# Kernel tuning notes

Hardware: AMD Instinct MI355X
Metric: run time of the kernel (lower is better)

Reference implementation:

```python
import jax, jax.numpy as jnp
import numpy as np
import math

B, S, E, H, F, L, V = 4, 256, 512, 8, 2048, 4, 32000
HD = E // H
MAXLEN = 5000  # EnhancedPositionalEncoding max_len default


def _ln(x, s, b):
    m = jnp.mean(x, axis=-1, keepdims=True)
    v = jnp.mean((x - m) ** 2, axis=-1, keepdims=True)
    return (x - m) / jnp.sqrt(v + 1e-5) * s + b


def setup_inputs() -> dict:
    key = jax.random.key(0)
    ks = jax.random.split(key, 10)
    n = lambda k, shape: jax.random.normal(k, shape, jnp.float32) * 0.02
    return {
        "src": jax.random.randint(ks[0], (B, S), 0, V),
        "emb": jax.random.uniform(ks[1], (V, E), jnp.float32, -0.1, 0.1),
        "rel_table": n(ks[2], (2 * MAXLEN - 1, E)),
        "norm_in_s": jnp.ones(E, jnp.float32), "norm_in_b": jnp.zeros(E, jnp.float32),
        "inW": n(ks[3], (L, 3 * E, E)), "inB": jnp.zeros((L, 3 * E), jnp.float32),
        "outW": n(ks[4], (L, E, E)), "outB": jnp.zeros((L, E), jnp.float32),
        "ln1_s": jnp.ones((L, E), jnp.float32), "ln1_b": jnp.zeros((L, E), jnp.float32),
        "ln2_s": jnp.ones((L, E), jnp.float32), "ln2_b": jnp.zeros((L, E), jnp.float32),
        "w1": n(ks[5], (L, F, E)), "b1": jnp.zeros((L, F), jnp.float32),
        "w2": n(ks[6], (L, E, F)), "b2": jnp.zeros((L, E), jnp.float32),
        "normf_s": jnp.ones(E, jnp.float32), "normf_b": jnp.zeros(E, jnp.float32),
        "dec_w": jax.random.uniform(ks[7], (V, E), jnp.float32, -0.1, 0.1),
        "dec_b": jnp.zeros(V, jnp.float32),
    }


def reference(src, emb, rel_table, norm_in_s, norm_in_b, inW, inB, outW, outB,
              ln1_s, ln1_b, ln2_s, ln2_b, w1, b1, w2, b2, normf_s, normf_b,
              dec_w, dec_b):
    x = emb[src] * math.sqrt(E)                 # [B,S,E], pos_encoder is identity in relative mode
    x = _ln(x, norm_in_s, norm_in_b)
    # relative-position embedding gather: idx[l,m] = (m - l) + S - 1
    pos = jnp.arange(S)
    rel_idx = (pos[None, :] - pos[:, None]) + S - 1
    rel = rel_table[rel_idx].reshape(S, S, H, HD)  # [S,S,H,hd]
    # NOTE: torch adds the BOOL triu mask to float scores -> +1.0 at masked positions
    mask = jnp.triu(jnp.ones((S, S), jnp.float32), 1)
    scale = 1.0 / math.sqrt(HD)
    for l in range(L):
        h = _ln(x, ln1_s[l], ln1_b[l])
        qkv = h @ inW[l].T + inB[l]
        q, k, v = jnp.split(qkv, 3, axis=-1)
        q = q.reshape(B, S, H, HD).transpose(0, 2, 1, 3)  # [B,H,S,hd]
        k = k.reshape(B, S, H, HD).transpose(0, 2, 1, 3)
        v = v.reshape(B, S, H, HD).transpose(0, 2, 1, 3)
        scores = jnp.einsum('bhqd,bhkd->bhqk', q, k) * scale
        bias = jnp.einsum('bhld,lmhd->bhlm', q, rel)      # relative-position bias (unscaled, as in torch)
        attn = jax.nn.softmax(scores + bias + mask, axis=-1)
        o = jnp.einsum('bhqk,bhkd->bhqd', attn, v).transpose(0, 2, 1, 3).reshape(B, S, E)
        x = x + (o @ outW[l].T + outB[l])
        h2 = _ln(x, ln2_s[l], ln2_b[l])
        ff = jax.nn.gelu(h2 @ w1[l].T + b1[l], approximate=False) @ w2[l].T + b2[l]
        x = x + ff
    x = _ln(x, normf_s, normf_b)  # encoder final norm
    return x @ dec_w.T + dec_b    # [B,S,V]
```

## Files before the change

kernel.cpp:

```cpp
#include <hip/hip_runtime.h>
#include <hip/hip_bf16.h>
#include <math.h>

#define BB 4
#define SS 256
#define EE 512
#define HH 8
#define HD 64
#define FFD 2048
#define LL 4
#define VV 32000
#define BS (BB*SS)
#define SQRT_E 22.627416997969522f
#define ATTN_SCALE 0.125f

typedef __bf16 bf16;
typedef __attribute__((ext_vector_type(4))) __bf16 bf16x4;
typedef __attribute__((ext_vector_type(8))) __bf16 bf16x8;
typedef __attribute__((ext_vector_type(4))) float f32x4;

#define GLOBAL_AS __attribute__((address_space(1)))
#define LDS_AS    __attribute__((address_space(3)))

__device__ __forceinline__ void load_lds16(const bf16* g, bf16* l) {
    __builtin_amdgcn_global_load_lds((const GLOBAL_AS unsigned int*)g,
                                     (LDS_AS unsigned int*)l, 16, 0, 0);
}

__global__ void cvt_all(const float* __restrict__ inW, const float* __restrict__ outW,
                        const float* __restrict__ w1, const float* __restrict__ w2,
                        const float* __restrict__ dec, const float* __restrict__ rel,
                        bf16* __restrict__ inWb, bf16* __restrict__ outWb,
                        bf16* __restrict__ w1b, bf16* __restrict__ w2b,
                        bf16* __restrict__ decb, bf16* __restrict__ relb,
                        const int* __restrict__ src, const float* __restrict__ emb,
                        const float* __restrict__ nsc, const float* __restrict__ nbi,
                        float* __restrict__ xout) {
    int b = blockIdx.x;
    int t = threadIdx.x;
    if (b >= 28544) {
        int row = b - 28544;
        const float* r = emb + (size_t)src[row] * EE;
        float v0 = r[t] * SQRT_E, v1 = r[t + 256] * SQRT_E;
        float sum = v0 + v1, sq = v0 * v0 + v1 * v1;
        #pragma unroll
        for (int off = 32; off; off >>= 1) {
            sum += __shfl_xor(sum, off);
            sq  += __shfl_xor(sq, off);
        }
        __shared__ float ssum[4], ssq[4];
        int wid = t >> 6, lane = t & 63;
        if (lane == 0) { ssum[wid] = sum; ssq[wid] = sq; }
        __syncthreads();
        sum = ssum[0] + ssum[1] + ssum[2] + ssum[3];
        sq  = ssq[0] + ssq[1] + ssq[2] + ssq[3];
        float mean = sum * (1.0f / EE);
        float var  = sq * (1.0f / EE) - mean * mean;
        float rstd = rsqrtf(var + 1e-5f);
        xout[(size_t)row * EE + t]       = (v0 - mean) * rstd * nsc[t] + nbi[t];
        xout[(size_t)row * EE + t + 256] = (v1 - mean) * rstd * nsc[t + 256] + nbi[t + 256];
        return;
    }
    const float* s; bf16* d; int base; int n;
    if (b < 3072)       { s = inW;  d = inWb;  base = b;         n = 3145728; }
    else if (b < 4096)  { s = outW; d = outWb; base = b - 3072;  n = 1048576; }
    else if (b < 8192)  { s = w1;   d = w1b;   base = b - 4096;  n = 4194304; }
    else if (b < 12288) { s = w2;   d = w2b;   base = b - 8192;  n = 4194304; }
    else if (b < 28288) { s = dec;  d = decb;  base = b - 12288; n = 16384000; }
    else                { s = rel;  d = relb;  base = b - 28288; n = 261632; }
    int i = (base * 256 + t) * 4;
    if (i < n) {
        float4 v = *(const float4*)(s + i);
        bf16x4 o;
        o[0] = (bf16)v.x; o[1] = (bf16)v.y; o[2] = (bf16)v.z; o[3] = (bf16)v.w;
        *(bf16x4*)(d + i) = o;
    }
}

template <typename OT>
__global__ void ln_kernel(const float* __restrict__ in, const float* __restrict__ sc,
                          const float* __restrict__ bi, OT* __restrict__ out) {
    int row = blockIdx.x;
    int t = threadIdx.x;
    const float* r = in + (size_t)row * EE;
    float v0 = r[t], v1 = r[t + 256];
    float sum = v0 + v1, sq = v0 * v0 + v1 * v1;
    #pragma unroll
    for (int off = 32; off; off >>= 1) {
        sum += __shfl_xor(sum, off);
        sq  += __shfl_xor(sq, off);
    }
    __shared__ float ssum[4], ssq[4];
    int wid = t >> 6, lane = t & 63;
    if (lane == 0) { ssum[wid] = sum; ssq[wid] = sq; }
    __syncthreads();
    sum = ssum[0] + ssum[1] + ssum[2] + ssum[3];
    sq  = ssq[0] + ssq[1] + ssq[2] + ssq[3];
    float mean = sum * (1.0f / EE);
    float var  = sq * (1.0f / EE) - mean * mean;
    float rstd = rsqrtf(var + 1e-5f);
    out[(size_t)row * EE + t]       = (OT)((v0 - mean) * rstd * sc[t] + bi[t]);
    out[(size_t)row * EE + t + 256] = (OT)((v1 - mean) * rstd * sc[t + 256] + bi[t + 256]);
}

__global__ void embed_ln_kernel(const int* __restrict__ src, const float* __restrict__ emb,
                                const float* __restrict__ sc, const float* __restrict__ bi,
                                float* __restrict__ out) {
    int row = blockIdx.x;
    int t = threadIdx.x;
    const float* r = emb + (size_t)src[row] * EE;
    float v0 = r[t] * SQRT_E, v1 = r[t + 256] * SQRT_E;
    float sum = v0 + v1, sq = v0 * v0 + v1 * v1;
    #pragma unroll
    for (int off = 32; off; off >>= 1) {
        sum += __shfl_xor(sum, off);
        sq  += __shfl_xor(sq, off);
    }
    __shared__ float ssum[4], ssq[4];
    int wid = t >> 6, lane = t & 63;
    if (lane == 0) { ssum[wid] = sum; ssq[wid] = sq; }
    __syncthreads();
    sum = ssum[0] + ssum[1] + ssum[2] + ssum[3];
    sq  = ssq[0] + ssq[1] + ssq[2] + ssq[3];
    float mean = sum * (1.0f / EE);
    float var  = sq * (1.0f / EE) - mean * mean;
    float rstd = rsqrtf(var + 1e-5f);
    out[(size_t)row * EE + t]       = (v0 - mean) * rstd * sc[t] + bi[t];
    out[(size_t)row * EE + t + 256] = (v1 - mean) * rstd * sc[t + 256] + bi[t + 256];
}

template <int BM, int BN, int MODE, int OBF16, int WRVT, int SWZ, int SPLITK>
__global__ __launch_bounds__(256) void gemm_bf16(
        const bf16* __restrict__ A, const bf16* __restrict__ W,
        const float* __restrict__ bias, void* __restrict__ Cout,
        const float* __restrict__ res, bf16* __restrict__ vT,
        int M, int N, int K) {
    constexpr int FM = BM / 32, FN = BN / 32;
    __shared__ bf16 Atile[2][BM * 32];
    __shared__ bf16 Btile[2][BN * 32];
    int tid = threadIdx.x;
    int wid = tid >> 6, lane = tid & 63;
    int wm = (wid >> 1) * (BM / 2), wn = (wid & 1) * (BN / 2);
    int bm, bn;
    if (SWZ) {
        int nbm = gridDim.x;
        int linear = blockIdx.y * nbm + blockIdx.x;
        int total = nbm * gridDim.y;
        int chunk = total >> 3;
        int xcd = linear & 7, idx = linear >> 3;
        int g = xcd * chunk + idx;
        bm = (g % nbm) * BM;
        bn = (g / nbm) * BN;
    } else {
        bm = blockIdx.x * BM;
        bn = blockIdx.y * BN;
    }
    int kp = (SPLITK > 1) ? blockIdx.z : 0;
    int kbeg = kp * (K / SPLITK);
    int kend = kbeg + K / SPLITK;

    f32x4 acc[FM][FN];
    #pragma unroll
    for (int i = 0; i < FM; i++)
        #pragma unroll
        for (int j = 0; j < FN; j++)
            acc[i][j] = (f32x4){0.f, 0.f, 0.f, 0.f};

    int mrow = lane & 15, kq = (lane >> 4) * 8;

    auto stage = [&](int buf, int k0) {
        #pragma unroll
        for (int it = 0; it < BM / 64; it++) {
            int c = it * 256 + tid;
            int row = c >> 2, kc = (c & 3) * 8;
            load_lds16(A + (size_t)(bm + row) * K + k0 + kc, &Atile[buf][c * 8]);
        }
        #pragma unroll
        for (int it = 0; it < BN / 64; it++) {
            int c = it * 256 + tid;
            int row = c >> 2, kc = (c & 3) * 8;
            load_lds16(W + (size_t)(bn + row) * K + k0 + kc, &Btile[buf][c * 8]);
        }
    };

    stage(0, kbeg);
    __syncthreads();
    int cur = 0;
    for (int k0 = kbeg; k0 < kend; k0 += 32) {
        if (k0 + 32 < kend) stage(cur ^ 1, k0 + 32);
        bf16x8 af[FM], bfv[FN];
        #pragma unroll
        for (int i = 0; i < FM; i++)
            af[i] = *(const bf16x8*)(&Atile[cur][(wm + i * 16 + mrow) * 32 + kq]);
        #pragma unroll
        for (int j = 0; j < FN; j++)
            bfv[j] = *(const bf16x8*)(&Btile[cur][(wn + j * 16 + mrow) * 32 + kq]);
        #pragma unroll
        for (int i = 0; i < FM; i++)
            #pragma unroll
            for (int j = 0; j < FN; j++)
                acc[i][j] = __builtin_amdgcn_mfma_f32_16x16x32_bf16(af[i], bfv[j], acc[i][j], 0, 0, 0);
        __syncthreads();
        cur ^= 1;
    }

    #pragma unroll
    for (int i = 0; i < FM; i++) {
        int row0 = bm + wm + i * 16 + (lane >> 4) * 4;
        #pragma unroll
        for (int j = 0; j < FN; j++) {
            int col = bn + wn + j * 16 + (lane & 15);
            float bv = bias[col];
            #pragma unroll
            for (int r = 0; r < 4; r++) {
                int row = row0 + r;
                if (SPLITK > 1) {
                    float v = acc[i][j][r];
                    if (kp == 0) v += bv;
                    atomicAdd((float*)Cout + (size_t)row * N + col, v);
                    continue;
                }
                float v = acc[i][j][r] + bv;
                if (MODE == 1) v = 0.5f * v * (1.0f + erff(v * 0.7071067811865476f));
                if (MODE == 2) v += res[(size_t)row * N + col];
                if (WRVT && col >= 1024) {
                    int cc = col - 1024;
                    vT[(size_t)(((row >> 8) * 8 + (cc >> 6)) * 64 + (cc & 63)) * 256 + (row & 255)] = (bf16)v;
                } else if (OBF16) ((bf16*)Cout)[(size_t)row * N + col] = (bf16)v;
                else              ((float*)Cout)[(size_t)row * N + col] = v;
            }
        }
    }
}

__global__ __launch_bounds__(256) void attn_mfma(const bf16* __restrict__ qkv,
        const bf16* __restrict__ relb, const bf16* __restrict__ vT,
        bf16* __restrict__ o) {
    int blk = blockIdx.x;
    int qt = blk & 3, bh = blk >> 2;
    int h = bh & 7, b = bh >> 3;
    int q0 = qt * 64, j0 = 192 - q0;
    int tid = threadIdx.x;
    int wid = tid >> 6, lane = tid & 63;
    int l15 = lane & 15, quad = lane >> 4;
    int mr0 = wid * 16;

    __shared__ __align__(16) bf16 Qs[64 * 72];
    __shared__ __align__(16) bf16 Stg[64 * 72];
    __shared__ __align__(16) bf16 BP[64 * 264];

    int c0 = tid, c1 = 256 + tid;
    int r0 = c0 >> 3, ch0 = (c0 & 7) * 8;
    int r1 = c1 >> 3, ch1 = (c1 & 7) * 8;

    const size_t qbase = (size_t)(b * 256 + q0) * 1536 + h * 64;
    *(bf16x8*)(Qs + r0 * 72 + ch0) = *(const bf16x8*)(qkv + qbase + (size_t)r0 * 1536 + ch0);
    *(bf16x8*)(Qs + r1 * 72 + ch1) = *(const bf16x8*)(qkv + qbase + (size_t)r1 * 1536 + ch1);

    bf16x8 pf0, pf1;
    {
        const size_t rb = (size_t)j0 * 512 + h * 64;
        pf0 = *(const bf16x8*)(relb + rb + (size_t)r0 * 512 + ch0);
        pf1 = *(const bf16x8*)(relb + rb + (size_t)r1 * 512 + ch1);
    }

    __syncthreads();
    bf16x8 af0 = *(const bf16x8*)(Qs + (mr0 + l15) * 72 + quad * 8);
    bf16x8 af1 = *(const bf16x8*)(Qs + (mr0 + l15) * 72 + 32 + quad * 8);

    f32x4 S[16];
    #pragma unroll
    for (int i = 0; i < 16; i++) S[i] = (f32x4){0.f, 0.f, 0.f, 0.f};

    for (int jc = 0; jc < 5; jc++) {
        *(bf16x8*)(Stg + r0 * 72 + ch0) = pf0;
        *(bf16x8*)(Stg + r1 * 72 + ch1) = pf1;
        __syncthreads();
        if (jc < 4) {
            const size_t rb = (size_t)(j0 + (jc + 1) * 64) * 512 + h * 64;
            pf0 = *(const bf16x8*)(relb + rb + (size_t)r0 * 512 + ch0);
            pf1 = *(const bf16x8*)(relb + rb + (size_t)r1 * 512 + ch1);
        } else {
            const size_t kb = (size_t)(b * 256) * 1536 + 512 + h * 64;
            pf0 = *(const bf16x8*)(qkv + kb + (size_t)r0 * 1536 + ch0);
            pf1 = *(const bf16x8*)(qkv + kb + (size_t)r1 * 1536 + ch1);
        }
        #pragma unroll
        for (int jt = 0; jt < 4; jt++) {
            f32x4 acc = (f32x4){0.f, 0.f, 0.f, 0.f};
            bf16x8 bv0 = *(const bf16x8*)(Stg + (jt * 16 + l15) * 72 + quad * 8);
            bf16x8 bv1 = *(const bf16x8*)(Stg + (jt * 16 + l15) * 72 + 32 + quad * 8);
            acc = __builtin_amdgcn_mfma_f32_16x16x32_bf16(af0, bv0, acc, 0, 0, 0);
            acc = __builtin_amdgcn_mfma_f32_16x16x32_bf16(af1, bv1, acc, 0, 0, 0);
            int jp = jc * 64 + jt * 16 + l15;
            #pragma unroll
            for (int r = 0; r < 4; r++) {
                int ll = mr0 + quad * 4 + r;
                int m = jp + ll - 63;
                if (m >= 0 && m < 256) BP[ll * 256 + m] = (bf16)acc[r];
            }
        }
        __syncthreads();
    }

    for (int kc = 0; kc < 4; kc++) {
        *(bf16x8*)(Stg + r0 * 72 + ch0) = pf0;
        *(bf16x8*)(Stg + r1 * 72 + ch1) = pf1;
        __syncthreads();
        if (kc < 3) {
            const size_t kb = (size_t)(b * 256 + (kc + 1) * 64) * 1536 + 512 + h * 64;
            pf0 = *(const bf16x8*)(qkv + kb + (size_t)r0 * 1536 + ch0);
            pf1 = *(const bf16x8*)(qkv + kb + (size_t)r1 * 1536 + ch1);
        } else {
            const size_t vb = (size_t)(bh * 64) * 256;
            pf0 = *(const bf16x8*)(vT + vb + (size_t)r0 * 256 + ch0);
            pf1 = *(const bf16x8*)(vT + vb + (size_t)r1 * 256 + ch1);
        }
        #pragma unroll
        for (int nt = 0; nt < 4; nt++) {
            bf16x8 bv0 = *(const bf16x8*)(Stg + (nt * 16 + l15) * 72 + quad * 8);
            bf16x8 bv1 = *(const bf16x8*)(Stg + (nt * 16 + l15) * 72 + 32 + quad * 8);
            S[kc * 4 + nt] = __builtin_amdgcn_mfma_f32_16x16x32_bf16(af0, bv0, S[kc * 4 + nt], 0, 0, 0);
            S[kc * 4 + nt] = __builtin_amdgcn_mfma_f32_16x16x32_bf16(af1, bv1, S[kc * 4 + nt], 0, 0, 0);
        }
        __syncthreads();
    }

    float rmax[4] = {-1e30f, -1e30f, -1e30f, -1e30f};
    #pragma unroll
    for (int T = 0; T < 16; T++) {
        int m = T * 16 + l15;
        #pragma unroll
        for (int r = 0; r < 4; r++) {
            int ll = mr0 + quad * 4 + r;
            float v = S[T][r] * ATTN_SCALE + (float)BP[ll * 256 + m]
                      + ((m > q0 + ll) ? 1.0f : 0.0f);
            S[T][r] = v;
            rmax[r] = fmaxf(rmax[r], v);
        }
    }
    #pragma unroll
    for (int r = 0; r < 4; r++)
        #pragma unroll
        for (int d = 1; d < 16; d <<= 1)
            rmax[r] = fmaxf(rmax[r], __shfl_xor(rmax[r], d));
    float rsum[4] = {0.f, 0.f, 0.f, 0.f};
    #pragma unroll
    for (int T = 0; T < 16; T++)
        #pragma unroll
        for (int r = 0; r < 4; r++) {
            float p = expf(S[T][r] - rmax[r]);
            S[T][r] = p;
            rsum[r] += p;
        }
    #pragma unroll
    for (int r = 0; r < 4; r++)
        #pragma unroll
        for (int d = 1; d < 16; d <<= 1)
            rsum[r] += __shfl_xor(rsum[r], d);

    __syncthreads();
    #pragma unroll
    for (int T = 0; T < 16; T++)
        #pragma unroll
        for (int r = 0; r < 4; r++)
            BP[(mr0 + quad * 4 + r) * 264 + T * 16 + l15] = (bf16)S[T][r];

    f32x4 oacc[4];
    #pragma unroll
    for (int i = 0; i < 4; i++) oacc[i] = (f32x4){0.f, 0.f, 0.f, 0.f};
    for (int kc = 0; kc < 4; kc++) {
        *(bf16x8*)(Stg + r0 * 72 + ch0) = pf0;
        *(bf16x8*)(Stg + r1 * 72 + ch1) = pf1;
        __syncthreads();
        if (kc < 3) {
            const size_t vb = (size_t)(bh * 64) * 256 + (kc + 1) * 64;
            pf0 = *(const bf16x8*)(vT + vb + (size_t)r0 * 256 + ch0);
            pf1 = *(const bf16x8*)(vT + vb + (size_t)r1 * 256 + ch1);
        }
        #pragma unroll
        for (int ks = 0; ks < 2; ks++) {
            bf16x8 ap = *(const bf16x8*)(BP + (mr0 + l15) * 264 + kc * 64 + ks * 32 + quad * 8);
            #pragma unroll
            for (int nt = 0; nt < 4; nt++) {
                bf16x8 bv = *(const bf16x8*)(Stg + (nt * 16 + l15) * 72 + ks * 32 + quad * 8);
                oacc[nt] = __builtin_amdgcn_mfma_f32_16x16x32_bf16(ap, bv, oacc[nt], 0, 0, 0);
            }
        }
        __syncthreads();
    }

    #pragma unroll
    for (int nt = 0; nt < 4; nt++)
        #pragma unroll
        for (int r = 0; r < 4; r++) {
            int ll = mr0 + quad * 4 + r;
            o[(size_t)(b * 256 + q0 + ll) * 512 + h * 64 + nt * 16 + l15] =
                (bf16)(oacc[nt][r] * (1.0f / rsum[r]));
        }
}

template <int MODE>
__global__ void gemm_nt(const float* __restrict__ A, const float* __restrict__ W,
                        const float* __restrict__ bias, float* __restrict__ C,
                        const float* __restrict__ res, int M, int N, int K) {
    __shared__ float As[64][17];
    __shared__ float Ws[64][17];
    int tid = threadIdx.x;
    int tx = tid & 15, ty = tid >> 4;
    int bm = blockIdx.y * 64, bn = blockIdx.x * 64;
    float acc[4][4] = {};
    for (int k0 = 0; k0 < K; k0 += 16) {
        #pragma unroll
        for (int i = 0; i < 4; i++) {
            int idx = tid + i * 256;
            int r = idx >> 4, c = idx & 15;
            As[r][c] = A[(size_t)(bm + r) * K + k0 + c];
            Ws[r][c] = W[(size_t)(bn + r) * K + k0 + c];
        }
        __syncthreads();
        #pragma unroll
        for (int kk = 0; kk < 16; kk++) {
            float a[4], w[4];
            #pragma unroll
            for (int i = 0; i < 4; i++) a[i] = As[ty * 4 + i][kk];
            #pragma unroll
            for (int j = 0; j < 4; j++) w[j] = Ws[tx * 4 + j][kk];
            #pragma unroll
            for (int i = 0; i < 4; i++)
                #pragma unroll
                for (int j = 0; j < 4; j++)
                    acc[i][j] += a[i] * w[j];
        }
        __syncthreads();
    }
    #pragma unroll
    for (int i = 0; i < 4; i++) {
        int row = bm + ty * 4 + i;
        #pragma unroll
        for (int j = 0; j < 4; j++) {
            int col = bn + tx * 4 + j;
            float v = acc[i][j] + bias[col];
            if (MODE == 1) v = 0.5f * v * (1.0f + erff(v * 0.7071067811865476f));
            if (MODE == 2) v += res[(size_t)row * N + col];
            C[(size_t)row * N + col] = v;
        }
    }
}

__global__ void attn_kernel(const float* __restrict__ qkv, const float* __restrict__ rel_table,
                            float* __restrict__ o) {
    int blk = blockIdx.x;
    int l = blk & (SS - 1);
    int bh = blk >> 8;
    int h = bh & (HH - 1);
    int b = bh >> 3;
    int t = threadIdx.x;
    int wid = t >> 6, lane = t & 63;

    __shared__ float qs[HD];
    __shared__ float attn_s[SS];
    __shared__ float swave[4];
    __shared__ float opart[4][HD];

    const float* qrow = qkv + (size_t)(b * SS + l) * (3 * EE) + h * HD;
    if (t < HD) qs[t] = qrow[t];
    __syncthreads();

    const float* krow   = qkv + (size_t)(b * SS + t) * (3 * EE) + EE + h * HD;
    const float* relrow = rel_table + (size_t)(t - l + SS - 1) * EE + h * HD;
    const float4* k4 = reinterpret_cast<const float4*>(krow);
    const float4* r4 = reinterpret_cast<const float4*>(relrow);
    float s1 = 0.f, s2 = 0.f;
    #pragma unroll
    for (int d4 = 0; d4 < HD / 4; d4++) {
        float4 kv = k4[d4], rv = r4[d4];
        float q0 = qs[4 * d4], q1 = qs[4 * d4 + 1], q2 = qs[4 * d4 + 2], q3 = qs[4 * d4 + 3];
        s1 += q0 * kv.x + q1 * kv.y + q2 * kv.z + q3 * kv.w;
        s2 += q0 * rv.x + q1 * rv.y + q2 * rv.z + q3 * rv.w;
    }
    float val = s1 * ATTN_SCALE + s2 + ((t > l) ? 1.0f : 0.0f);

    float m = val;
    #pragma unroll
    for (int off = 32; off; off >>= 1) m = fmaxf(m, __shfl_xor(m, off));
    if (lane == 0) swave[wid] = m;
    __syncthreads();
    m = fmaxf(fmaxf(swave[0], swave[1]), fmaxf(swave[2], swave[3]));
    float p = expf(val - m);
    float s = p;
    #pragma unroll
    for (int off = 32; off; off >>= 1) s += __shfl_xor(s, off);
    __syncthreads();
    if (lane == 0) swave[wid] = s;
    __syncthreads();
    float tot = swave[0] + swave[1] + swave[2] + swave[3];
    attn_s[t] = p;
    __syncthreads();

    int d = t & 63, part = t >> 6;
    const float* vbase = qkv + (size_t)(b * SS) * (3 * EE) + 2 * EE + h * HD + d;
    float acc = 0.f;
    int m0 = part * 64;
    #pragma unroll 8
    for (int mm = m0; mm < m0 + 64; mm++)
        acc += attn_s[mm] * vbase[(size_t)mm * (3 * EE)];
    opart[part][d] = acc;
    __syncthreads();
    if (t < 64) {
        float ov = (opart[0][d] + opart[1][d] + opart[2][d] + opart[3][d]) / tot;
        o[(size_t)(b * SS + l) * EE + h * HD + d] = ov;
    }
}

extern "C" void kernel_launch(void* const* d_in, const int* in_sizes, int n_in,
                              void* d_out, int out_size, void* d_ws, size_t ws_size,
                              hipStream_t stream) {
    const int*   src    = (const int*)  d_in[0];
    const float* emb    = (const float*)d_in[1];
    const float* rel    = (const float*)d_in[2];
    const float* nin_s  = (const float*)d_in[3];
    const float* nin_b  = (const float*)d_in[4];
    const float* inW    = (const float*)d_in[5];
    const float* inB    = (const float*)d_in[6];
    const float* outW   = (const float*)d_in[7];
    const float* outB   = (const float*)d_in[8];
    const float* ln1_s  = (const float*)d_in[9];
    const float* ln1_b  = (const float*)d_in[10];
    const float* ln2_s  = (const float*)d_in[11];
    const float* ln2_b  = (const float*)d_in[12];
    const float* w1     = (const float*)d_in[13];
    const float* b1     = (const float*)d_in[14];
    const float* w2     = (const float*)d_in[15];
    const float* b2     = (const float*)d_in[16];
    const float* normf_s= (const float*)d_in[17];
    const float* normf_b= (const float*)d_in[18];
    const float* dec_w  = (const float*)d_in[19];
    const float* dec_b  = (const float*)d_in[20];
    float* out = (float*)d_out;

    const size_t n_inW  = (size_t)LL * 3 * EE * EE;
    const size_t n_outW = (size_t)LL * EE * EE;
    const size_t n_w1   = (size_t)LL * FFD * EE;
    const size_t n_w2   = (size_t)LL * EE * FFD;
    const size_t n_dec  = (size_t)VV * EE;

    float* x    = (float*)d_ws;
    bf16*  qkvb = (bf16*)(x + (size_t)BS * EE);
    bf16*  hb   = qkvb + (size_t)BS * 3 * EE;
    bf16*  ob   = hb + (size_t)BS * EE;
    bf16*  ffb  = ob + (size_t)BS * EE;
    bf16*  vTb  = ffb + (size_t)BS * FFD;
    bf16*  relb = vTb + (size_t)BS * 512;
    bf16*  inWb  = relb + (size_t)512 * EE;
    bf16*  outWb = inWb + n_inW;
    bf16*  w1b   = outWb + n_outW;
    bf16*  w2b   = w1b + n_w1;
    bf16*  decWb = w2b + n_w2;
    size_t needed = (size_t)((char*)(decWb + n_dec) - (char*)d_ws);

    if (ws_size >= needed) {
        cvt_all<<<29568, 256, 0, stream>>>(inW, outW, w1, w2, dec_w, rel,
                                           inWb, outWb, w1b, w2b, decWb, relb,
                                           src, emb, nin_s, nin_b, x);

        for (int l = 0; l < LL; l++) {
            ln_kernel<bf16><<<BS, 256, 0, stream>>>(x, ln1_s + l * EE, ln1_b + l * EE, hb);
            gemm_bf16<64, 64, 0, 1, 1, 1, 1><<<dim3(BS / 64, 3 * EE / 64), 256, 0, stream>>>(
                hb, inWb + (size_t)l * 3 * EE * EE, inB + (size_t)l * 3 * EE, qkvb, nullptr,
                vTb, BS, 3 * EE, EE);
            attn_mfma<<<BB * HH * 4, 256, 0, stream>>>(qkvb, relb, vTb, ob);
            gemm_bf16<64, 64, 2, 0, 0, 1, 2><<<dim3(BS / 64, EE / 64, 2), 256, 0, stream>>>(
                ob, outWb + (size_t)l * EE * EE, outB + (size_t)l * EE, x, x,
                nullptr, BS, EE, EE);
            ln_kernel<bf16><<<BS, 256, 0, stream>>>(x, ln2_s + l * EE, ln2_b + l * EE, hb);
            gemm_bf16<64, 64, 1, 1, 0, 1, 1><<<dim3(BS / 64, FFD / 64), 256, 0, stream>>>(
                hb, w1b + (size_t)l * FFD * EE, b1 + (size_t)l * FFD, ffb, nullptr,
                nullptr, BS, FFD, EE);
            gemm_bf16<64, 64, 2, 0, 0, 1, 4><<<dim3(BS / 64, EE / 64, 4), 256, 0, stream>>>(
                ffb, w2b + (size_t)l * EE * FFD, b2 + (size_t)l * EE, x, x,
                nullptr, BS, EE, FFD);
        }

        ln_kernel<bf16><<<BS, 256, 0, stream>>>(x, normf_s, normf_b, hb);
        gemm_bf16<128, 128, 0, 0, 0, 1, 1><<<dim3(BS / 128, VV / 128), 256, 0, stream>>>(
            hb, decWb, dec_b, out, nullptr, nullptr, BS, VV, EE);
    } else {
        float* h     = x + (size_t)BS * EE;
        float* qkvf  = h + (size_t)BS * EE;
        float* o     = qkvf + (size_t)BS * 3 * EE;
        float* ffmid = o + (size_t)BS * EE;

        embed_ln_kernel<<<BS, 256, 0, stream>>>(src, emb, nin_s, nin_b, x);
        for (int l = 0; l < LL; l++) {
            ln_kernel<float><<<BS, 256, 0, stream>>>(x, ln1_s + l * EE, ln1_b + l * EE, h);
            gemm_nt<0><<<dim3(3 * EE / 64, BS / 64), 256, 0, stream>>>(
                h, inW + (size_t)l * 3 * EE * EE, inB + (size_t)l * 3 * EE, qkvf, nullptr,
                BS, 3 * EE, EE);
            attn_kernel<<<BB * HH * SS, 256, 0, stream>>>(qkvf, rel, o);
            gemm_nt<2><<<dim3(EE / 64, BS / 64), 256, 0, stream>>>(
                o, outW + (size_t)l * EE * EE, outB + (size_t)l * EE, x, x,
                BS, EE, EE);
            ln_kernel<float><<<BS, 256, 0, stream>>>(x, ln2_s + l * EE, ln2_b + l * EE, h);
            gemm_nt<1><<<dim3(FFD / 64, BS / 64), 256, 0, stream>>>(
                h, w1 + (size_t)l * FFD * EE, b1 + (size_t)l * FFD, ffmid, nullptr,
                BS, FFD, EE);
            gemm_nt<2><<<dim3(EE / 64, BS / 64), 256, 0, stream>>>(
                ffmid, w2 + (size_t)l * EE * FFD, b2 + (size_t)l * EE, x, x,
                BS, EE, FFD);
        }
        ln_kernel<float><<<BS, 256, 0, stream>>>(x, normf_s, normf_b, h);
        gemm_nt<0><<<dim3(VV / 64, BS / 64), 256, 0, stream>>>(
            h, dec_w, dec_b, out, nullptr, BS, VV, EE);
    }
}
```

Baseline: 584.7 us.

## Replace LDS-tiled GEMMs in layer loop with direct global-load MFMA kernel

Adds a gemm_direct kernel that loads A and W fragments straight from global memory into registers and issues bf16 MFMAs, with no shared-memory staging or barriers. The K loop is fully unrolled over a compile-time span. All four per-layer GEMMs (QKV, out-proj, FFN1, FFN2) now use it, while the decoder GEMM keeps the tiled kernel. The aim is to cut LDS traffic and sync overhead on these small GEMMs. In exchange, each wave re-reads operands from global/L2 with no data reuse, and the accesses are strided per lane.

```diff
diff --git a/kernel.cpp b/kernel.cpp
--- a/kernel.cpp
+++ b/kernel.cpp
@@ -127,6 +127,74 @@
     float rstd = rsqrtf(var + 1e-5f);
     out[(size_t)row * EE + t]       = (v0 - mean) * rstd * sc[t] + bi[t];
     out[(size_t)row * EE + t + 256] = (v1 - mean) * rstd * sc[t + 256] + bi[t + 256];
+}
+
+template <int KSPAN, int MODE, int OBF16, int WRVT, int SPLITK>
+__global__ __launch_bounds__(256, 2) void gemm_direct(
+        const bf16* __restrict__ A, const bf16* __restrict__ W,
+        const float* __restrict__ bias, void* __restrict__ Cout,
+        const float* __restrict__ res, bf16* __restrict__ vT,
+        int M, int N, int K) {
+    int tid = threadIdx.x;
+    int wid = tid >> 6, lane = tid & 63;
+    int wm = (wid >> 1) * 32, wn = (wid & 1) * 32;
+    int mrow = lane & 15, kq = (lane >> 4) * 8;
+    int bm = blockIdx.x * 64, bn = blockIdx.y * 64;
+    int kp = (SPLITK > 1) ? blockIdx.z : 0;
+    int kbeg = kp * KSPAN;
+
+    const bf16* Ar0 = A + (size_t)(bm + wm + mrow) * K + kbeg + kq;
+    const bf16* Ar1 = Ar0 + (size_t)16 * K;
+    const bf16* Wr0 = W + (size_t)(bn + wn + mrow) * K + kbeg + kq;
+    const bf16* Wr1 = Wr0 + (size_t)16 * K;
+
+    f32x4 acc[2][2];
+    #pragma unroll
+    for (int i = 0; i < 2; i++)
+        #pragma unroll
+        for (int j = 0; j < 2; j++)
+            acc[i][j] = (f32x4){0.f, 0.f, 0.f, 0.f};
+
+    #pragma unroll
+    for (int ks = 0; ks < KSPAN / 32; ks++) {
+        int k = ks * 32;
+        bf16x8 a0 = *(const bf16x8*)(Ar0 + k);
+        bf16x8 a1 = *(const bf16x8*)(Ar1 + k);
+        bf16x8 b0 = *(const bf16x8*)(Wr0 + k);
+        bf16x8 b1 = *(const bf16x8*)(Wr1 + k);
+        acc[0][0] = __builtin_amdgcn_mfma_f32_16x16x32_bf16(a0, b0, acc[0][0], 0, 0, 0);
+        acc[0][1] = __builtin_amdgcn_mfma_f32_16x16x32_bf16(a0, b1, acc[0][1], 0, 0, 0);
+        acc[1][0] = __builtin_amdgcn_mfma_f32_16x16x32_bf16(a1, b0, acc[1][0], 0, 0, 0);
+        acc[1][1] = __builtin_amdgcn_mfma_f32_16x16x32_bf16(a1, b1, acc[1][1], 0, 0, 0);
+    }
+
+    #pragma unroll
+    for (int i = 0; i < 2; i++) {
+        int row0 = bm + wm + i * 16 + (lane >> 4) * 4;
+        #pragma unroll
+        for (int j = 0; j < 2; j++) {
+            int col = bn + wn + j * 16 + (lane & 15);
+            float bv = bias[col];
+            #pragma unroll
+            for (int r = 0; r < 4; r++) {
+                int row = row0 + r;
+                if (SPLITK > 1) {
+                    float v = acc[i][j][r];
+                    if (kp == 0) v += bv;
+                    atomicAdd((float*)Cout + (size_t)row * N + col, v);
+                    continue;
+                }
+                float v = acc[i][j][r] + bv;
+                if (MODE == 1) v = 0.5f * v * (1.0f + erff(v * 0.7071067811865476f));
+                if (MODE == 2) v += res[(size_t)row * N + col];
+                if (WRVT && col >= 1024) {
+                    int cc = col - 1024;
+                    vT[(size_t)(((row >> 8) * 8 + (cc >> 6)) * 64 + (cc & 63)) * 256 + (row & 255)] = (bf16)v;
+                } else if (OBF16) ((bf16*)Cout)[(size_t)row * N + col] = (bf16)v;
+                else              ((float*)Cout)[(size_t)row * N + col] = v;
+            }
+        }
+    }
 }
 
 template <int BM, int BN, int MODE, int OBF16, int WRVT, int SWZ, int SPLITK>
@@ -566,18 +634,18 @@
 
         for (int l = 0; l < LL; l++) {
             ln_kernel<bf16><<<BS, 256, 0, stream>>>(x, ln1_s + l * EE, ln1_b + l * EE, hb);
-            gemm_bf16<64, 64, 0, 1, 1, 1, 1><<<dim3(BS / 64, 3 * EE / 64), 256, 0, stream>>>(
+            gemm_direct<512, 0, 1, 1, 1><<<dim3(BS / 64, 3 * EE / 64), 256, 0, stream>>>(
                 hb, inWb + (size_t)l * 3 * EE * EE, inB + (size_t)l * 3 * EE, qkvb, nullptr,
                 vTb, BS, 3 * EE, EE);
             attn_mfma<<<BB * HH * 4, 256, 0, stream>>>(qkvb, relb, vTb, ob);
-            gemm_bf16<64, 64, 2, 0, 0, 1, 2><<<dim3(BS / 64, EE / 64, 2), 256, 0, stream>>>(
+            gemm_direct<256, 2, 0, 0, 2><<<dim3(BS / 64, EE / 64, 2), 256, 0, stream>>>(
                 ob, outWb + (size_t)l * EE * EE, outB + (size_t)l * EE, x, x,
                 nullptr, BS, EE, EE);
             ln_kernel<bf16><<<BS, 256, 0, stream>>>(x, ln2_s + l * EE, ln2_b + l * EE, hb);
-            gemm_bf16<64, 64, 1, 1, 0, 1, 1><<<dim3(BS / 64, FFD / 64), 256, 0, stream>>>(
+            gemm_direct<512, 1, 1, 0, 1><<<dim3(BS / 64, FFD / 64), 256, 0, stream>>>(
                 hb, w1b + (size_t)l * FFD * EE, b1 + (size_t)l * FFD, ffb, nullptr,
                 nullptr, BS, FFD, EE);
-            gemm_bf16<64, 64, 2, 0, 0, 1, 4><<<dim3(BS / 64, EE / 64, 4), 256, 0, stream>>>(
+            gemm_direct<512, 2, 0, 0, 4><<<dim3(BS / 64, EE / 64, 4), 256, 0, stream>>>(
                 ffb, w2b + (size_t)l * EE * FFD, b2 + (size_t)l * EE, x, x,
                 nullptr, BS, EE, FFD);
         }
```

Measured after the change: 663.0 us. 13.4% more time.
